# Optimization experiments

Measured on AMD Instinct MI355X. Metric: run time of the kernel, lower is better.

## Reference

```python
import jax, jax.numpy as jnp
import numpy as np

SEQ, NV, NH, NR = 32768, 256, 512, 256


def _bern(key, p):
    # torch.bernoulli: sample is non-differentiable
    return (jax.random.uniform(key, p.shape, dtype=p.dtype) < p).astype(p.dtype)


def setup_inputs() -> dict:
    key = jax.random.key(0)
    ks = jax.random.split(key, 8)
    f32 = jnp.float32
    return {
        "v_seq": (jax.random.uniform(ks[0], (SEQ, NV), dtype=f32) < 0.1).astype(f32),
        "W1": jax.random.normal(ks[1], (NV, NH), dtype=f32) * 0.01,
        "bv": jnp.zeros((NV,), f32),
        "bh1": jnp.zeros((NH,), f32),
        "W2": jax.random.normal(ks[2], (NH, NH), dtype=f32) * 0.01,
        "bh2": jnp.zeros((NH,), f32),
        "Wyv": jax.random.normal(ks[3], (NV, NR), dtype=f32) * 1e-4,
        "Wyh1": jax.random.normal(ks[4], (NH, NR), dtype=f32) * 1e-4,
        "Wyh2": jax.random.normal(ks[5], (NH, NR), dtype=f32) * 1e-4,
        "Wvu": jax.random.normal(ks[6], (NV, NR), dtype=f32) * 0.01,
        "Wuu": jax.random.normal(ks[7], (NR, NR), dtype=f32) * 0.01,
        "bu": jnp.zeros((NR,), f32),
        "k": 5,
    }


def reference(v_seq, W1, bv, bh1, W2, bh2, Wyv, Wyh1, Wyh2, Wvu, Wuu, bu, k):
    dtype = v_seq.dtype
    nr = Wuu.shape[0]
    seq_len = v_seq.shape[0]

    # vanilla tanh RNN (abstract _run_rnn in base class)
    def rnn_step(u, v):
        u_new = jnp.tanh(v @ Wvu + u @ Wuu + bu)
        return u_new, u_new

    _, rnn_out = jax.lax.scan(rnn_step, jnp.zeros((nr,), dtype), v_seq)
    shifted = jnp.concatenate([jnp.zeros((1, nr), dtype), rnn_out[:-1]], axis=0)

    bv_t = bv + shifted @ Wyv.T    # [S, NV]
    bh1_t = bh1 + shifted @ Wyh1.T  # [S, NH]
    bh2_t = bh2 + shifted @ Wyh2.T  # [S, NH]

    key = jax.random.key(42)

    # CD-k Gibbs chain, RBM1 (visible <-> hidden1)
    v_sample = v_seq
    mean_v = None
    for _ in range(k):
        key, k1, k2 = jax.random.split(key, 3)
        h = _bern(k1, jax.nn.sigmoid(v_sample @ W1 + bh1_t))
        mean_v = jax.nn.sigmoid(h @ W1.T + bv_t)
        v_sample = _bern(k2, mean_v)

    def free_energy1(v):
        return -(v * bv_t).sum(-1) - jax.nn.softplus(v @ W1 + bh1_t).sum(-1)

    cost1 = (free_energy1(v_seq) - free_energy1(jax.lax.stop_gradient(v_sample))).mean()

    # CD-k Gibbs chain, RBM2 (hidden1 <-> hidden2)
    h1 = jax.nn.sigmoid(v_seq @ W1 + bh1_t)
    h1_sample = h1
    for _ in range(k):
        key, k1, k2 = jax.random.split(key, 3)
        h2 = _bern(k1, jax.nn.sigmoid(h1_sample @ W2 + bh2_t))
        h1_sample = _bern(k2, jax.nn.sigmoid(h2 @ W2.T + bh1_t))

    def free_energy2(h):
        return -(h * bh1_t).sum(-1) - jax.nn.softplus(h @ W2 + bh2_t).sum(-1)

    cost2 = (free_energy2(h1) - free_energy2(jax.lax.stop_gradient(h1_sample))).mean()

    eps = 1e-10
    monitor = (v_seq * jnp.log(mean_v + eps)
               + (1.0 - v_seq) * jnp.log(1.0 - mean_v + eps)).sum() / seq_len
    return (cost1 + cost2, monitor)
```

## Files before the change

### kernel.cpp

```cpp
#include <hip/hip_runtime.h>
#include <cstdint>

#define S_LEN 32768
#define NV 256
#define NH 512
#define NR 256

typedef short bf16x8 __attribute__((ext_vector_type(8)));
typedef float f32x4 __attribute__((ext_vector_type(4)));
typedef unsigned short ushort_t;

__device__ __forceinline__ float b2f(ushort_t u) {
  return __uint_as_float(((uint32_t)u) << 16);
}
__device__ __forceinline__ ushort_t f2b(float f) {
  uint32_t x = __float_as_uint(f);
  uint32_t r = (x + 0x7fffu + ((x >> 16) & 1u)) >> 16;
  return (ushort_t)r;
}

#define GLOAD_LDS16(gsrc, ldst)                                        \
  __builtin_amdgcn_global_load_lds(                                    \
      (const __attribute__((address_space(1))) void*)(gsrc),           \
      (__attribute__((address_space(3))) void*)(ldst), 16, 0, 0)

#define TFR(x0,x1,r) { x0 += x1; x1 = ((x1 << (r)) | (x1 >> (32 - (r)))); x1 ^= x0; }
__host__ __forceinline__ void tf2x32(uint32_t k0, uint32_t k1,
                                     uint32_t x0, uint32_t x1,
                                     uint32_t* o0, uint32_t* o1) {
  uint32_t k2 = k0 ^ k1 ^ 0x1BD11BDAu;
  x0 += k0; x1 += k1;
  TFR(x0,x1,13) TFR(x0,x1,15) TFR(x0,x1,26) TFR(x0,x1,6)
  x0 += k1; x1 += k2 + 1u;
  TFR(x0,x1,17) TFR(x0,x1,29) TFR(x0,x1,16) TFR(x0,x1,24)
  x0 += k2; x1 += k0 + 2u;
  TFR(x0,x1,13) TFR(x0,x1,15) TFR(x0,x1,26) TFR(x0,x1,6)
  x0 += k0; x1 += k1 + 3u;
  TFR(x0,x1,17) TFR(x0,x1,29) TFR(x0,x1,16) TFR(x0,x1,24)
  x0 += k1; x1 += k2 + 4u;
  TFR(x0,x1,13) TFR(x0,x1,15) TFR(x0,x1,26) TFR(x0,x1,6)
  x0 += k2; x1 += k0 + 5u;
  *o0 = x0; *o1 = x1;
}

__device__ __forceinline__ float fast_uniform(uint32_t k0, uint32_t k1, uint32_t idx) {
  uint32_t h = idx ^ k0;
  h *= 0xCC9E2D51u; h = (h << 15) | (h >> 17); h *= 0x1B873593u;
  h ^= k1;
  h ^= h >> 16; h *= 0x85EBCA6Bu;
  h ^= h >> 13; h *= 0xC2B2AE35u;
  h ^= h >> 16;
  return __uint_as_float((h >> 9) | 0x3f800000u) - 1.0f;
}

__device__ __forceinline__ float wave_reduce(float v) {
#pragma unroll
  for (int o = 32; o > 0; o >>= 1) v += __shfl_down(v, o, 64);
  return v;
}
__device__ __forceinline__ float softplusf(float z) {
  return fmaxf(z, 0.f) + log1pf(expf(-fabsf(z)));
}

#define F_SAMP  4
#define F_H1    8
#define F_FE    16
#define F_MON   32
#define F_DOTB  64
#define F_DOTS  128

struct GemmArgs {
  const ushort_t* A;
  const ushort_t* BT;
  int boff;
  ushort_t* C;
  ushort_t* C2;
  const float* vseqf;
  double* fe_acc;
  double* mon_acc;
  float sign;
  uint32_t rk0, rk1;
  int N, K, nbx;
};

template<int FLAGS>
__device__ __forceinline__ void run_gemm(const GemmArgs& g,
                                         const ushort_t* __restrict__ biasm, int ldb,
                                         ushort_t* __restrict__ As0,
                                         ushort_t* __restrict__ As1,
                                         ushort_t* __restrict__ Bs0,
                                         ushort_t* __restrict__ Bs1) {
  const int tid = threadIdx.x;
  const int lane = tid & 63, wave = tid >> 6;
  const int wm = wave >> 1, wn = wave & 1;
  const int q = lane >> 4, l16 = lane & 15;
  const int m0 = blockIdx.y * 128, n0 = blockIdx.x * 128;
  const int N = g.N, K = g.K;

  f32x4 acc[4][4];
#pragma unroll
  for (int mt = 0; mt < 4; mt++)
#pragma unroll
    for (int nt = 0; nt < 4; nt++) {
      const int gn = n0 + wn * 64 + nt * 16 + l16;
      const int gmb = m0 + wm * 64 + mt * 16 + q * 4;
#pragma unroll
      for (int rg = 0; rg < 4; rg++)
        acc[mt][nt][rg] = b2f(biasm[(size_t)(gmb + rg) * ldb + g.boff + gn]);
    }

  auto stage = [&](ushort_t* As, ushort_t* Bs, int kk) {
#pragma unroll
    for (int j = 0; j < 4; j++) {
      int c = j * 256 + tid;
      int r = c >> 3, bl = c & 7, bg = bl ^ (r & 7);
      const int ldso = (j * 256 + wave * 64) * 8;
      GLOAD_LDS16(&g.A[(size_t)(m0 + r) * K + kk + bg * 8], &As[ldso]);
      GLOAD_LDS16(&g.BT[(size_t)(n0 + r) * K + kk + bg * 8], &Bs[ldso]);
    }
  };
  auto compute = [&](const ushort_t* As, const ushort_t* Bs) {
#pragma unroll
    for (int c = 0; c < 2; c++) {
      bf16x8 af[4], bf[4];
#pragma unroll
      for (int mt = 0; mt < 4; mt++) {
        int r = wm * 64 + mt * 16 + l16;
        af[mt] = *(const bf16x8*)&As[r * 64 + (((c * 4 + q) ^ (r & 7)) * 8)];
      }
#pragma unroll
      for (int nt = 0; nt < 4; nt++) {
        int r = wn * 64 + nt * 16 + l16;
        bf[nt] = *(const bf16x8*)&Bs[r * 64 + (((c * 4 + q) ^ (r & 7)) * 8)];
      }
#pragma unroll
      for (int mt = 0; mt < 4; mt++)
#pragma unroll
        for (int nt = 0; nt < 4; nt++)
          acc[mt][nt] = __builtin_amdgcn_mfma_f32_16x16x32_bf16(
              af[mt], bf[nt], acc[mt][nt], 0, 0, 0);
    }
  };

  stage(As0, Bs0, 0);
  __syncthreads();
  for (int kk = 0; kk < K; kk += 128) {
    stage(As1, Bs1, kk + 64);
    compute(As0, Bs0);
    __syncthreads();
    if (kk + 128 < K) stage(As0, Bs0, kk + 128);
    compute(As1, Bs1);
    __syncthreads();
  }

  float fe_sum = 0.f, mon_sum = 0.f;
#pragma unroll
  for (int mt = 0; mt < 4; mt++) {
#pragma unroll
    for (int nt = 0; nt < 4; nt++) {
      const int gn = n0 + wn * 64 + nt * 16 + l16;
      const int gmb = m0 + wm * 64 + mt * 16 + q * 4;
#pragma unroll
      for (int rg = 0; rg < 4; rg++) {
        const int gm = gmb + rg;
        const size_t idx = (size_t)gm * N + gn;
        float z = acc[mt][nt][rg];
        float be = 0.f;
        if constexpr (FLAGS & (F_DOTB | F_DOTS))
          be = b2f(biasm[(size_t)gm * ldb + g.boff + gn]);
        if constexpr (FLAGS & (F_SAMP | F_H1 | F_MON)) {
          float e = __expf(-z);
          if constexpr (FLAGS & F_SAMP) {
            float uu = fast_uniform(g.rk0, g.rk1, (uint32_t)idx);
            bool sbit = fmaf(uu, e, uu) < 1.f;
            g.C[idx] = sbit ? (ushort_t)0x3f80 : (ushort_t)0;
            if constexpr (FLAGS & F_DOTS) fe_sum += sbit ? be : 0.f;
          }
          if constexpr (FLAGS & (F_H1 | F_MON)) {
            float pp = __builtin_amdgcn_rcpf(1.f + e);
            if constexpr (FLAGS & F_H1) g.C2[idx] = f2b(pp);
            if constexpr (FLAGS & F_DOTB) fe_sum += pp * be;
            if constexpr (FLAGS & F_MON) {
              float v = g.vseqf[idx];
              mon_sum += (v != 0.f) ? logf(pp + 1e-10f) : logf(1.f - pp + 1e-10f);
            }
          }
        }
        if constexpr (FLAGS & F_FE) fe_sum += softplusf(z);
      }
    }
  }
  if constexpr (FLAGS & (F_FE | F_DOTB | F_DOTS)) {
    float s = wave_reduce(fe_sum);
    if (lane == 0) atomicAdd(g.fe_acc, (double)(-g.sign * s));
  }
  if constexpr (FLAGS & F_MON) {
    float s = wave_reduce(mon_sum);
    if (lane == 0) atomicAdd(g.mon_acc, (double)s);
  }
}

template<int FLAGS>
__global__ __launch_bounds__(256)
void gemm_samp(GemmArgs g, const ushort_t* __restrict__ biasm, int ldb) {
  __shared__ ushort_t As0[128 * 64], As1[128 * 64];
  __shared__ ushort_t Bs0[128 * 64], Bs1[128 * 64];
  if ((int)blockIdx.x >= g.nbx) return;
  run_gemm<FLAGS>(g, biasm, ldb, As0, As1, Bs0, Bs1);
}

template<int F0, int F1>
__global__ __launch_bounds__(256)
void gemm_pair(GemmArgs g0, GemmArgs g1, const ushort_t* __restrict__ biasm, int ldb) {
  __shared__ ushort_t As0[128 * 64], As1[128 * 64];
  __shared__ ushort_t Bs0[128 * 64], Bs1[128 * 64];
  if (blockIdx.z == 0) {
    if ((int)blockIdx.x >= g0.nbx) return;
    run_gemm<F0>(g0, biasm, ldb, As0, As1, Bs0, Bs1);
  } else {
    if ((int)blockIdx.x >= g1.nbx) return;
    run_gemm<F1>(g1, biasm, ldb, As0, As1, Bs0, Bs1);
  }
}

template<bool OUTF32, bool VDOT>
__global__ __launch_bounds__(256)
void gemm_bias(const ushort_t* __restrict__ A, const ushort_t* __restrict__ BT,
               const float* __restrict__ biasv, ushort_t* __restrict__ Cb,
               float* __restrict__ Cf, const float* __restrict__ vdata,
               double* __restrict__ dacc, int M, int N, int K) {
  __shared__ ushort_t As0[128 * 64], As1[128 * 64];
  __shared__ ushort_t Bs0[128 * 64], Bs1[128 * 64];
  const int tid = threadIdx.x;
  const int lane = tid & 63, wave = tid >> 6;
  const int wm = wave >> 1, wn = wave & 1;
  const int q = lane >> 4, l16 = lane & 15;
  const int m0 = blockIdx.y * 128, n0 = blockIdx.x * 128;

  f32x4 acc[4][4];
#pragma unroll
  for (int i = 0; i < 4; i++)
#pragma unroll
    for (int j = 0; j < 4; j++) acc[i][j] = (f32x4){0.f, 0.f, 0.f, 0.f};

  auto stage = [&](ushort_t* As, ushort_t* Bs, int kk) {
#pragma unroll
    for (int j = 0; j < 4; j++) {
      int c = j * 256 + tid;
      int r = c >> 3, bl = c & 7, bg = bl ^ (r & 7);
      const int ldso = (j * 256 + wave * 64) * 8;
      GLOAD_LDS16(&A[(size_t)(m0 + r) * K + kk + bg * 8], &As[ldso]);
      GLOAD_LDS16(&BT[(size_t)(n0 + r) * K + kk + bg * 8], &Bs[ldso]);
    }
  };
  auto compute = [&](const ushort_t* As, const ushort_t* Bs) {
#pragma unroll
    for (int c = 0; c < 2; c++) {
      bf16x8 af[4], bf[4];
#pragma unroll
      for (int mt = 0; mt < 4; mt++) {
        int r = wm * 64 + mt * 16 + l16;
        af[mt] = *(const bf16x8*)&As[r * 64 + (((c * 4 + q) ^ (r & 7)) * 8)];
      }
#pragma unroll
      for (int nt = 0; nt < 4; nt++) {
        int r = wn * 64 + nt * 16 + l16;
        bf[nt] = *(const bf16x8*)&Bs[r * 64 + (((c * 4 + q) ^ (r & 7)) * 8)];
      }
#pragma unroll
      for (int mt = 0; mt < 4; mt++)
#pragma unroll
        for (int nt = 0; nt < 4; nt++)
          acc[mt][nt] = __builtin_amdgcn_mfma_f32_16x16x32_bf16(
              af[mt], bf[nt], acc[mt][nt], 0, 0, 0);
    }
  };

  stage(As0, Bs0, 0);
  __syncthreads();
  for (int kk = 0; kk < K; kk += 128) {
    stage(As1, Bs1, kk + 64);
    compute(As0, Bs0);
    __syncthreads();
    if (kk + 128 < K) stage(As0, Bs0, kk + 128);
    compute(As1, Bs1);
    __syncthreads();
  }

  float dsum = 0.f;
#pragma unroll
  for (int mt = 0; mt < 4; mt++)
#pragma unroll
    for (int nt = 0; nt < 4; nt++) {
      const int gn = n0 + wn * 64 + nt * 16 + l16;
      const int gmb = m0 + wm * 64 + mt * 16 + q * 4;
      const float bvv = biasv[gn];
#pragma unroll
      for (int rg = 0; rg < 4; rg++) {
        const size_t idx = (size_t)(gmb + rg) * N + gn;
        float z = acc[mt][nt][rg] + bvv;
        if constexpr (OUTF32) Cf[idx] = z; else Cb[idx] = f2b(z);
        if constexpr (VDOT)
          if (n0 < 256) dsum += z * vdata[(size_t)(gmb + rg) * 256 + gn];
      }
    }
  if constexpr (VDOT) {
    if (n0 < 256) {
      float s = wave_reduce(dsum);
      if ((tid & 63) == 0) atomicAdd(dacc, (double)(-s));
    }
  }
}

__global__ __launch_bounds__(1024, 1)
void rnn_scan(const float* __restrict__ Apre, const float* __restrict__ Wuu,
              ushort_t* __restrict__ shifted) {
  const int tid = threadIdx.x;
  const int j = tid >> 2;
  const int s = tid & 3;
  const int t_begin = blockIdx.x * 128;
  const int t_end = t_begin + 128;
  const int t0 = (t_begin >= 16) ? (t_begin - 16) : 0;

  float w[64];
#pragma unroll
  for (int i = 0; i < 64; i++) w[i] = Wuu[(size_t)(s * 64 + i) * 256 + j];

  __shared__ float u[2][280];
  __shared__ float asg[32 * 256];
  if (tid < 256) u[0][(tid >> 6) * 68 + (tid & 63)] = 0.f;
  if (blockIdx.x == 0 && s == 0) shifted[j] = 0;
  __syncthreads();

  const int jp = (j >> 6) * 68 + (j & 63);
  int p = 0;
  for (int tb = t0; tb < t_end; tb += 32) {
    int srow = tb + (tid >> 5);
    if (srow >= S_LEN) srow = S_LEN - 1;
    int scol = (tid & 31) * 8;
    float4 a0 = *(const float4*)&Apre[(size_t)srow * 256 + scol];
    float4 a1 = *(const float4*)&Apre[(size_t)srow * 256 + scol + 4];
    *(float4*)&asg[(tid >> 5) * 256 + scol] = a0;
    *(float4*)&asg[(tid >> 5) * 256 + scol + 4] = a1;
    __syncthreads();
#pragma unroll 1
    for (int i = 0; i < 32; i++) {
      const int t = tb + i;
      if (t >= t_end) break;
      float p0 = 0.f, p1 = 0.f, p2 = 0.f, p3 = 0.f;
#pragma unroll
      for (int qq = 0; qq < 64; qq += 4) {
        float4 uv = *(const float4*)&u[p][s * 68 + qq];
        p0 = fmaf(uv.x, w[qq + 0], p0);
        p1 = fmaf(uv.y, w[qq + 1], p1);
        p2 = fmaf(uv.z, w[qq + 2], p2);
        p3 = fmaf(uv.w, w[qq + 3], p3);
      }
      float ps = (p0 + p1) + (p2 + p3);
      ps += __shfl_xor(ps, 1, 64);
      ps += __shfl_xor(ps, 2, 64);
      float z = asg[i * 256 + j] + ps;
      float e = __expf(2.f * z);
      float unew = 1.f - 2.f * __builtin_amdgcn_rcpf(e + 1.f);
      if (s == 0) {
        u[1 - p][jp] = unew;
        if (t >= t_begin && (t + 1) < S_LEN)
          shifted[(size_t)(t + 1) * 256 + j] = f2b(unew);
      }
      __syncthreads();
      p ^= 1;
    }
  }
}

__global__ __launch_bounds__(256)
void prep_all(const float* __restrict__ v_seq, ushort_t* __restrict__ vseq_bf,
              const float* __restrict__ Wyv, const float* __restrict__ Wyh1,
              const float* __restrict__ Wyh2, ushort_t* __restrict__ Wycat,
              const float* __restrict__ W1, ushort_t* __restrict__ BTw1t,
              ushort_t* __restrict__ BTw1,
              const float* __restrict__ W2, ushort_t* __restrict__ BTw2t,
              ushort_t* __restrict__ BTw2,
              const float* __restrict__ Wvu, ushort_t* __restrict__ BTwvu,
              const float* __restrict__ bv, const float* __restrict__ bh1,
              const float* __restrict__ bh2, float* __restrict__ bveccat) {
  int b = blockIdx.x;
  const int tid = threadIdx.x;
  if (b < 32768) { int i = b * 256 + tid; vseq_bf[i] = f2b(v_seq[i]); return; }
  b -= 32768;
  if (b < 256)  { int i = b * 256 + tid; Wycat[i] = f2b(Wyv[i]); return; }
  b -= 256;
  if (b < 512)  { int i = b * 256 + tid; Wycat[65536 + i] = f2b(Wyh1[i]); return; }
  b -= 512;
  if (b < 512)  { int i = b * 256 + tid; Wycat[196608 + i] = f2b(Wyh2[i]); return; }
  b -= 512;
  if (b < 512)  { int i = b * 256 + tid; BTw1t[i] = f2b(W1[i]); return; }
  b -= 512;
  if (b < 1024) { int i = b * 256 + tid; BTw2t[i] = f2b(W2[i]); return; }
  b -= 1024;
  if (b < 256)  { int i = b * 256 + tid; int r = i >> 8, c = i & 255;
                  BTwvu[c * 256 + r] = f2b(Wvu[i]); return; }
  b -= 256;
  if (b < 512)  { int i = b * 256 + tid; int r = i >> 9, c = i & 511;
                  BTw1[(size_t)c * 256 + r] = f2b(W1[i]); return; }
  b -= 512;
  if (b < 1024) { int i = b * 256 + tid; int r = i >> 9, c = i & 511;
                  BTw2[(size_t)c * 512 + r] = f2b(W2[i]); return; }
  b -= 1024;
  { int i = b * 256 + tid;
    if (i < 1280)
      bveccat[i] = (i < 256) ? bv[i] : (i < 768) ? bh1[i - 256] : bh2[i - 768]; }
}

__global__ void finalize_kernel(const double* __restrict__ acc, float* __restrict__ out) {
  out[0] = (float)(acc[0] / (double)S_LEN);
  out[1] = (float)(acc[1] / (double)S_LEN);
}

extern "C" void kernel_launch(void* const* d_in, const int* in_sizes, int n_in,
                              void* d_out, int out_size, void* d_ws, size_t ws_size,
                              hipStream_t stream) {
  (void)in_sizes; (void)n_in; (void)out_size; (void)ws_size;
  const float* v_seq = (const float*)d_in[0];
  const float* W1    = (const float*)d_in[1];
  const float* bv    = (const float*)d_in[2];
  const float* bh1   = (const float*)d_in[3];
  const float* W2    = (const float*)d_in[4];
  const float* bh2   = (const float*)d_in[5];
  const float* Wyv   = (const float*)d_in[6];
  const float* Wyh1  = (const float*)d_in[7];
  const float* Wyh2  = (const float*)d_in[8];
  const float* Wvu   = (const float*)d_in[9];
  const float* Wuu   = (const float*)d_in[10];
  const float* bu    = (const float*)d_in[11];
  float* out = (float*)d_out;

  const size_t SN = (size_t)S_LEN * NV;
  const size_t SH = (size_t)S_LEN * NH;
  const int NB = NV + NH + NH;
  char* base = (char*)d_ws;
  size_t cur = 0;
  auto take = [&](size_t bytes) { size_t o = cur; cur += (bytes + 255) & ~(size_t)255; return o; };
  double*   acc      = (double*)  (base + take(64));
  ushort_t* BTwvu    = (ushort_t*)(base + take(65536 * 2));
  ushort_t* Wycat    = (ushort_t*)(base + take((size_t)NB * NR * 2));
  float*    bveccat  = (float*)   (base + take(NB * 4));
  ushort_t* BTw1     = (ushort_t*)(base + take(131072 * 2));
  ushort_t* BTw1t    = (ushort_t*)(base + take(131072 * 2));
  ushort_t* BTw2     = (ushort_t*)(base + take(262144 * 2));
  ushort_t* BTw2t    = (ushort_t*)(base + take(262144 * 2));
  ushort_t* vseq_bf  = (ushort_t*)(base + take(SN * 2));
  ushort_t* shifted  = (ushort_t*)(base + take(SN * 2));
  ushort_t* bias_cat = (ushort_t*)(base + take((size_t)S_LEN * NB * 2));
  ushort_t* h1buf    = (ushort_t*)(base + take(SH * 2));
  ushort_t* sampA    = (ushort_t*)(base + take(SH * 2));
  ushort_t* sampB    = (ushort_t*)(base + take(SN * 2));
  ushort_t* sampC    = (ushort_t*)(base + take(SH * 2));
  ushort_t* sampD = h1buf;
  float* Arnn = (float*)bias_cat;

  uint32_t ka[20], kb[20];
  uint32_t K0 = 0u, K1 = 42u;
  for (int it = 0; it < 10; it++) {
    uint32_t n0, n1, a0, a1, b0, b1;
    tf2x32(K0, K1, 0u, 0u, &n0, &n1);
    tf2x32(K0, K1, 0u, 1u, &a0, &a1);
    tf2x32(K0, K1, 0u, 2u, &b0, &b1);
    ka[2 * it] = a0; kb[2 * it] = a1;
    ka[2 * it + 1] = b0; kb[2 * it + 1] = b1;
    K0 = n0; K1 = n1;
  }

  hipMemsetAsync(acc, 0, 2 * sizeof(double), stream);

  dim3 blk(256);
  prep_all<<<dim3(37381), blk, 0, stream>>>(
      v_seq, vseq_bf, Wyv, Wyh1, Wyh2, Wycat, W1, BTw1t, BTw1,
      W2, BTw2t, BTw2, Wvu, BTwvu, bv, bh1, bh2, bveccat);

  const int M = S_LEN;
  gemm_bias<true, false><<<dim3(2, M / 128), blk, 0, stream>>>(
      vseq_bf, BTwvu, bu, nullptr, Arnn, nullptr, nullptr, M, NV, NV);
  rnn_scan<<<dim3(S_LEN / 128), dim3(1024), 0, stream>>>(Arnn, Wuu, shifted);
  gemm_bias<false, true><<<dim3(NB / 128, M / 128), blk, 0, stream>>>(
      shifted, Wycat, bveccat, bias_cat, nullptr, v_seq, acc, M, NB, NR);

  const int OFF_BV = 0, OFF_BH1 = NV, OFF_BH2 = NV + NH;
  auto mk = [&](const ushort_t* A, const ushort_t* BT, int boff, ushort_t* C,
                ushort_t* C2, const float* vs, float sign, int key, int N, int K) {
    GemmArgs g;
    g.A = A; g.BT = BT; g.boff = boff;
    g.C = C; g.C2 = C2; g.vseqf = vs;
    g.fe_acc = acc; g.mon_acc = acc + 1; g.sign = sign;
    g.rk0 = key >= 0 ? ka[key] : 0; g.rk1 = key >= 0 ? kb[key] : 0;
    g.N = N; g.K = K; g.nbx = N / 128;
    return g;
  };

  gemm_samp<F_SAMP | F_H1 | F_FE | F_DOTB>
      <<<dim3(4, M / 128), blk, 0, stream>>>(
      mk(vseq_bf, BTw1, OFF_BH1, sampA, h1buf, nullptr, 1.0f, 0, NH, NV),
      bias_cat, NB);

  dim3 pg(4, M / 128, 2);
  GemmArgs V[5], Hh[4], A2g[5], B2g[5];
  for (int it = 0; it < 5; it++) {
    if (it > 0)
      Hh[it - 1] = mk(sampB, BTw1, OFF_BH1, sampA, nullptr, nullptr, 0.f,
                      2 * it, NH, NV);
    V[it] = mk(sampA, BTw1t, OFF_BV, sampB, nullptr,
               (it == 4) ? v_seq : nullptr, (it == 4) ? -1.0f : 0.f,
               2 * it + 1, NV, NH);
    A2g[it] = mk((it == 0) ? h1buf : sampD,
                 BTw2, OFF_BH2, sampC, nullptr, nullptr,
                 (it == 0) ? 1.0f : 0.f, 10 + 2 * it, NH, NH);
    B2g[it] = mk(sampC, BTw2t, OFF_BH1, sampD, nullptr, nullptr,
                 (it == 4) ? -1.0f : 0.f, 11 + 2 * it, NH, NH);
  }
  GemmArgs FE1 = mk(sampB, BTw1, OFF_BH1, nullptr, nullptr, nullptr, -1.0f,
                    -1, NH, NV);
  GemmArgs FE2 = mk(sampD, BTw2, OFF_BH2, nullptr, nullptr, nullptr, -1.0f,
                    -1, NH, NH);

  gemm_pair<F_SAMP, F_SAMP | F_FE>
      <<<pg, blk, 0, stream>>>(V[0], A2g[0], bias_cat, NB);
  gemm_pair<F_SAMP, F_SAMP>
      <<<pg, blk, 0, stream>>>(Hh[0], B2g[0], bias_cat, NB);
  gemm_pair<F_SAMP, F_SAMP>
      <<<pg, blk, 0, stream>>>(V[1], A2g[1], bias_cat, NB);
  gemm_pair<F_SAMP, F_SAMP>
      <<<pg, blk, 0, stream>>>(Hh[1], B2g[1], bias_cat, NB);
  gemm_pair<F_SAMP, F_SAMP>
      <<<pg, blk, 0, stream>>>(V[2], A2g[2], bias_cat, NB);
  gemm_pair<F_SAMP, F_SAMP>
      <<<pg, blk, 0, stream>>>(Hh[2], B2g[2], bias_cat, NB);
  gemm_pair<F_SAMP, F_SAMP>
      <<<pg, blk, 0, stream>>>(V[3], A2g[3], bias_cat, NB);
  gemm_pair<F_SAMP, F_SAMP>
      <<<pg, blk, 0, stream>>>(Hh[3], B2g[3], bias_cat, NB);
  gemm_pair<F_SAMP | F_MON | F_DOTS, F_SAMP>
      <<<pg, blk, 0, stream>>>(V[4], A2g[4], bias_cat, NB);
  gemm_pair<F_FE, F_SAMP | F_DOTS>
      <<<pg, blk, 0, stream>>>(FE1, B2g[4], bias_cat, NB);

  gemm_samp<F_FE><<<dim3(4, M / 128), blk, 0, stream>>>(FE2, bias_cat, NB);

  finalize_kernel<<<1, 1, 0, stream>>>(acc, out);
}
```

Measured before the change: 1.378 ms.

## Fuse RNN-conditioned bias GEMM into sampling GEMMs and halve hash calls

Instead of reading a precomputed per-row bias matrix to initialize accumulators, each sampling GEMM now extends its K loop by 256 and multiplies the shifted RNN state by the bias projection weights inline, then adds the static bias vector. It also derives two 16-bit uniforms from each 32-bit hash, so the hash is computed half as often. This trades bias-matrix loads at init for extra MFMA work (K grows from 256/512 by 256) in every Gibbs GEMM, and lowers uniform resolution to 16 bits. The bias matrix is still read in epilogues with dot flags.

```diff
diff --git a/kernel.cpp b/kernel.cpp
--- a/kernel.cpp
+++ b/kernel.cpp
@@ -43,14 +43,14 @@
   *o0 = x0; *o1 = x1;
 }
 
-__device__ __forceinline__ float fast_uniform(uint32_t k0, uint32_t k1, uint32_t idx) {
+__device__ __forceinline__ uint32_t fast_hash(uint32_t k0, uint32_t k1, uint32_t idx) {
   uint32_t h = idx ^ k0;
   h *= 0xCC9E2D51u; h = (h << 15) | (h >> 17); h *= 0x1B873593u;
   h ^= k1;
   h ^= h >> 16; h *= 0x85EBCA6Bu;
   h ^= h >> 13; h *= 0xC2B2AE35u;
   h ^= h >> 16;
-  return __uint_as_float((h >> 9) | 0x3f800000u) - 1.0f;
+  return h;
 }
 
 __device__ __forceinline__ float wave_reduce(float v) {
@@ -72,6 +72,9 @@
 struct GemmArgs {
   const ushort_t* A;
   const ushort_t* BT;
+  const ushort_t* Ax;
+  const ushort_t* BXT;
+  const float* bvec;
   int boff;
   ushort_t* C;
   ushort_t* C2;
@@ -96,27 +99,25 @@
   const int q = lane >> 4, l16 = lane & 15;
   const int m0 = blockIdx.y * 128, n0 = blockIdx.x * 128;
   const int N = g.N, K = g.K;
+  const int KT = K + 256;
 
   f32x4 acc[4][4];
 #pragma unroll
   for (int mt = 0; mt < 4; mt++)
 #pragma unroll
-    for (int nt = 0; nt < 4; nt++) {
-      const int gn = n0 + wn * 64 + nt * 16 + l16;
-      const int gmb = m0 + wm * 64 + mt * 16 + q * 4;
-#pragma unroll
-      for (int rg = 0; rg < 4; rg++)
-        acc[mt][nt][rg] = b2f(biasm[(size_t)(gmb + rg) * ldb + g.boff + gn]);
-    }
-
-  auto stage = [&](ushort_t* As, ushort_t* Bs, int kk) {
+    for (int nt = 0; nt < 4; nt++) acc[mt][nt] = (f32x4){0.f, 0.f, 0.f, 0.f};
+
+  auto stage = [&](ushort_t* As, ushort_t* Bs, int kks) {
+    const ushort_t* Ap; const ushort_t* Bp; size_t lda, ldbt; int k0;
+    if (kks < K) { Ap = g.A;  Bp = g.BT;  lda = (size_t)K; ldbt = (size_t)K; k0 = kks; }
+    else         { Ap = g.Ax; Bp = g.BXT; lda = 256;       ldbt = 256;       k0 = kks - K; }
 #pragma unroll
     for (int j = 0; j < 4; j++) {
       int c = j * 256 + tid;
       int r = c >> 3, bl = c & 7, bg = bl ^ (r & 7);
       const int ldso = (j * 256 + wave * 64) * 8;
-      GLOAD_LDS16(&g.A[(size_t)(m0 + r) * K + kk + bg * 8], &As[ldso]);
-      GLOAD_LDS16(&g.BT[(size_t)(n0 + r) * K + kk + bg * 8], &Bs[ldso]);
+      GLOAD_LDS16(&Ap[(size_t)(m0 + r) * lda + k0 + bg * 8], &As[ldso]);
+      GLOAD_LDS16(&Bp[(size_t)(n0 + r) * ldbt + k0 + bg * 8], &Bs[ldso]);
     }
   };
   auto compute = [&](const ushort_t* As, const ushort_t* Bs) {
@@ -144,11 +145,11 @@
 
   stage(As0, Bs0, 0);
   __syncthreads();
-  for (int kk = 0; kk < K; kk += 128) {
+  for (int kk = 0; kk < KT; kk += 128) {
     stage(As1, Bs1, kk + 64);
     compute(As0, Bs0);
     __syncthreads();
-    if (kk + 128 < K) stage(As0, Bs0, kk + 128);
+    if (kk + 128 < KT) stage(As0, Bs0, kk + 128);
     compute(As1, Bs1);
     __syncthreads();
   }
@@ -160,18 +161,27 @@
     for (int nt = 0; nt < 4; nt++) {
       const int gn = n0 + wn * 64 + nt * 16 + l16;
       const int gmb = m0 + wm * 64 + mt * 16 + q * 4;
+      const float bvv = g.bvec[gn];
+      uint32_t h0 = 0, h1 = 0;
+      if constexpr (FLAGS & F_SAMP) {
+        uint32_t pb = (uint32_t)((gmb >> 1) * N + gn);
+        h0 = fast_hash(g.rk0, g.rk1, pb);
+        h1 = fast_hash(g.rk0, g.rk1, pb + (uint32_t)N);
+      }
 #pragma unroll
       for (int rg = 0; rg < 4; rg++) {
         const int gm = gmb + rg;
         const size_t idx = (size_t)gm * N + gn;
-        float z = acc[mt][nt][rg];
+        float z = acc[mt][nt][rg] + bvv;
         float be = 0.f;
         if constexpr (FLAGS & (F_DOTB | F_DOTS))
           be = b2f(biasm[(size_t)gm * ldb + g.boff + gn]);
         if constexpr (FLAGS & (F_SAMP | F_H1 | F_MON)) {
           float e = __expf(-z);
           if constexpr (FLAGS & F_SAMP) {
-            float uu = fast_uniform(g.rk0, g.rk1, (uint32_t)idx);
+            uint32_t hb = (rg & 2) ? h1 : h0;
+            uint32_t ub = (rg & 1) ? (hb >> 16) : (hb & 0xffffu);
+            float uu = (float)ub * (1.0f / 65536.0f);
             bool sbit = fmaf(uu, e, uu) < 1.f;
             g.C[idx] = sbit ? (ushort_t)0x3f80 : (ushort_t)0;
             if constexpr (FLAGS & F_DOTS) fe_sum += sbit ? be : 0.f;
@@ -490,6 +500,9 @@
                 ushort_t* C2, const float* vs, float sign, int key, int N, int K) {
     GemmArgs g;
     g.A = A; g.BT = BT; g.boff = boff;
+    g.Ax = shifted;
+    g.BXT = Wycat + (size_t)boff * 256;
+    g.bvec = bveccat + boff;
     g.C = C; g.C2 = C2; g.vseqf = vs;
     g.fe_acc = acc; g.mon_acc = acc + 1; g.sign = sign;
     g.rk0 = key >= 0 ? ka[key] : 0; g.rk1 = key >= 0 ? kb[key] : 0;
```

Result: slower. 1.453 ms (+5.5%).
